# Performance work log

Hardware: AMD Instinct MI355X
Metric: run time of the kernel (lower is better)

Reference implementation:

```python
import jax, jax.numpy as jnp
import numpy as np

B, T, H, OUT_LEN, D_IN, D_OUT = 512, 512, 256, 8, 64, 64

def _lstm_seq(x, Wih, Whh, bih, bhh):
    # batch_first LSTM, zero initial state; x: [B,T,D] -> [B,T,H]
    b = bih + bhh
    h0 = jnp.zeros((x.shape[0], Whh.shape[1]), x.dtype)
    def step(carry, xt):
        h, c = carry
        g = xt @ Wih.T + h @ Whh.T + b
        i, f, gg, o = jnp.split(g, 4, axis=-1)  # torch gate order i,f,g,o
        c = jax.nn.sigmoid(f) * c + jax.nn.sigmoid(i) * jnp.tanh(gg)
        h = jax.nn.sigmoid(o) * jnp.tanh(c)
        return (h, c), h
    _, hs = jax.lax.scan(step, (h0, h0), jnp.swapaxes(x, 0, 1))
    return jnp.swapaxes(hs, 0, 1)

def _lstm_cell0(xt, Wih, bih, bhh):
    # single decode step; original calls self.dec with fresh zero (h,c) each
    # step, so the recurrent matrix Whh never contributes.
    g = xt @ Wih.T + bih + bhh
    i, f, gg, o = jnp.split(g, 4, axis=-1)
    c = jax.nn.sigmoid(i) * jnp.tanh(gg)
    return jax.nn.sigmoid(o) * jnp.tanh(c)

def _mlp(x, Ws, bs, Wl, bl):
    # simple.mlp: hidden Linear+ReLU stack, linear output (dropout off)
    for k in range(Ws.shape[0]):
        x = jax.nn.relu(x @ Ws[k] + bs[k])
    return x @ Wl + bl

def setup_inputs():
    key = jax.random.key(0)
    ks = iter(jax.random.split(key, 32))
    def W(shape, fan):
        return jax.random.normal(next(ks), shape, jnp.float32) / np.float32(np.sqrt(fan))
    return {
        'x': jax.random.normal(next(ks), (B, T, D_IN), jnp.float32),
        'in_W': W((D_IN, H), D_IN), 'in_b': jnp.zeros((H,), jnp.float32),
        'enc_Wih': W((4*H, H), H), 'enc_Whh': W((4*H, H), H),
        'enc_bih': jnp.zeros((4*H,), jnp.float32), 'enc_bhh': jnp.zeros((4*H,), jnp.float32),
        'dec_Wih': W((4*H, 2*H), 2*H), 'dec_Whh': W((4*H, H), H),
        'dec_bih': jnp.zeros((4*H,), jnp.float32), 'dec_bhh': jnp.zeros((4*H,), jnp.float32),
        'w_Ws': W((3, H, H), H), 'w_bs': jnp.zeros((3, H), jnp.float32), 'w_Wl': W((H, H), H), 'w_bl': jnp.zeros((H,), jnp.float32),
        'u_Ws': W((3, H, H), H), 'u_bs': jnp.zeros((3, H), jnp.float32), 'u_Wl': W((H, H), H), 'u_bl': jnp.zeros((H,), jnp.float32),
        'v_Ws': W((7, H, H), H), 'v_bs': jnp.zeros((7, H), jnp.float32), 'v_Wl': W((H, 1), H), 'v_bl': jnp.zeros((1,), jnp.float32),
        'out_W': W((H, D_OUT), H), 'out_b': jnp.zeros((D_OUT,), jnp.float32),
    }

def reference(x, in_W, in_b, enc_Wih, enc_Whh, enc_bih, enc_bhh,
              dec_Wih, dec_Whh, dec_bih, dec_bhh,
              w_Ws, w_bs, w_Wl, w_bl, u_Ws, u_bs, u_Wl, u_bl,
              v_Ws, v_bs, v_Wl, v_bl, out_W, out_b):
    h = x @ in_W + in_b                                       # input projection [B,T,H]
    enc = _lstm_seq(h, enc_Wih, enc_Whh, enc_bih, enc_bhh)    # [B,T,H]
    whs = _mlp(enc, w_Ws, w_bs, w_Wl, w_bl)                   # w(hs), loop-invariant (hoisted)
    def dec_step(s, _):
        us = _mlp(s, u_Ws, u_bs, u_Wl, u_bl)                  # [B,H]
        e = _mlp(jnp.tanh(us[:, None, :] + whs), v_Ws, v_bs, v_Wl, v_bl)  # [B,T,1]
        a = jax.nn.softmax(e, axis=1)                         # softmax over time
        c_t = jnp.sum(a * enc, axis=1)                        # [B,H] weighted sum
        s_new = _lstm_cell0(jnp.concatenate([c_t, s], axis=-1), dec_Wih, dec_bih, dec_bhh)
        return s_new, s_new
    s0 = jnp.zeros((x.shape[0], H), x.dtype)
    _, ss = jax.lax.scan(dec_step, s0, None, length=OUT_LEN)  # [OUT_LEN,B,H]
    dec = jnp.swapaxes(ss, 0, 1)                              # [B,OUT_LEN,H]
    return dec @ out_W + out_b                                # output projection
```

## Files before the change

kernel.cpp:

```cpp
#include <hip/hip_runtime.h>
#include <math.h>

#define B_    512
#define T_    512
#define H_    256
#define DIN_  64
#define OL_   8
#define DOUT_ 64

#define CBv   128
#define HSTR  32768

typedef unsigned short u16;
typedef unsigned int u32;
typedef unsigned long long ull;
typedef __attribute__((ext_vector_type(8))) short short8;
typedef __attribute__((ext_vector_type(4))) float f32x4;

static __device__ __forceinline__ float sigm(float x){ return 1.0f/(1.0f + expf(-x)); }
static __device__ __forceinline__ float bf2f(u16 h){
  u32 u = ((u32)h) << 16; float f; __builtin_memcpy(&f, &u, 4); return f;
}
static __device__ __forceinline__ u16 f2bf(float f){
  u32 u; __builtin_memcpy(&u, &f, 4);
  u = (u + 0x7fffu + ((u >> 16) & 1u)) >> 16;
  return (u16)u;
}
static __device__ __forceinline__ u32 packhl(float f){
  u16 h = f2bf(f);
  u16 lo = f2bf(f - bf2f(h));
  return ((u32)h << 16) | (u32)lo;
}
static __device__ __forceinline__ float unpackhl(u32 w){
  return bf2f((u16)(w >> 16)) + bf2f((u16)(w & 0xffff));
}
static __device__ __forceinline__ u32 al(const u32* p){
  return __hip_atomic_load(p, __ATOMIC_RELAXED, __HIP_MEMORY_SCOPE_AGENT);
}
static __device__ __forceinline__ void as_(u32* p, u32 v){
  __hip_atomic_store(p, v, __ATOMIC_RELAXED, __HIP_MEMORY_SCOPE_AGENT);
}

__global__ void k_wpt(const float* __restrict__ inW, const float* __restrict__ Wih,
                      float* __restrict__ WpT)
{
  int gid = blockIdx.x * 256 + threadIdx.x;
  int c = gid >> 6, d = gid & 63;
  const float* wr = Wih + c * H_;
  const float* ir = inW + d * H_;
  float acc = 0.f;
  #pragma unroll 4
  for (int e = 0; e < H_; e += 4) {
    float4 av = *(const float4*)(ir + e);
    float4 bv = *(const float4*)(wr + e);
    acc += av.x*bv.x + av.y*bv.y + av.z*bv.z + av.w*bv.w;
  }
  WpT[c*64 + d] = acc;
}

__global__ void k_bp(const float* __restrict__ inb, const float* __restrict__ Wih,
                     const float* __restrict__ bih, const float* __restrict__ bhh,
                     float* __restrict__ bp)
{
  int c = blockIdx.x * 256 + threadIdx.x;
  const float* wr = Wih + c * H_;
  float acc = bih[c] + bhh[c];
  for (int e = 0; e < H_; ++e) acc += inb[e] * wr[e];
  bp[c] = acc;
}

__global__ void k_dwt(const float* __restrict__ dWih, float* __restrict__ dWt)
{
  int gid = blockIdx.x * 256 + threadIdx.x;
  int j = gid >> 9, k = gid & 511;
  int row = (j < 256) ? j : (j + 256);
  dWt[k*768 + j] = dWih[row*512 + k];
}

__global__ void k_wall(const float* __restrict__ wWs, const float* __restrict__ wWl,
                       const float* __restrict__ uWs, const float* __restrict__ uWl,
                       const float* __restrict__ vWs, u16* __restrict__ outb)
{
  int lyr = blockIdx.y;
  const float* W = (lyr < 3)  ? wWs + lyr*65536
                 : (lyr == 3) ? wWl
                 : (lyr < 7)  ? uWs + (lyr-4)*65536
                 : (lyr == 7) ? uWl
                 :              vWs + (lyr-8)*65536;
  u16* out = outb + (size_t)lyr*131072;
  int gid = blockIdx.x * 256 + threadIdx.x;
  int k = gid & 255, n = gid >> 8;
  float v = W[k*256 + n];
  int s = k >> 5, j = k & 7;
  int lane = (((k >> 3) & 3) << 4) | (n & 15);
  int fl = ((s*16) + (n >> 4))*512 + lane*8 + j;
  u16 h = f2bf(v);
  out[fl] = h;
  out[65536 + fl] = f2bf(v - bf2f(h));
}

__global__ void k_whhfl(const float* __restrict__ Whh, u16* __restrict__ out)
{
  int gid = blockIdx.x * 256 + threadIdx.x;
  int j = gid & 7, l = (gid >> 3) & 63, ctg = (gid >> 9) & 63, s = gid >> 15;
  int k = s*32 + (l >> 4)*8 + j;
  int wv = ctg >> 2, g = ctg & 3;
  int row = g*256 + wv*16 + (l & 15);
  float v = Whh[row*256 + k];
  int fl = (s*64 + ctg)*512 + l*8 + j;
  u16 h = f2bf(v);
  out[fl] = h;
  out[262144 + fl] = f2bf(v - bf2f(h));
}

__global__ void k_wpfl(const float* __restrict__ WpT, u16* __restrict__ out)
{
  int gid = blockIdx.x * 256 + threadIdx.x;
  int j = gid & 7, l = (gid >> 3) & 63, ctg = (gid >> 9) & 63, s = gid >> 15;
  int k = s*32 + (l >> 4)*8 + j;
  int wv = ctg >> 2, g = ctg & 3;
  int row = g*256 + wv*16 + (l & 15);
  float v = WpT[row*64 + k];
  int fl = (s*64 + ctg)*512 + l*8 + j;
  u16 h = f2bf(v);
  out[fl] = h;
  out[65536 + fl] = f2bf(v - bf2f(h));
}

__global__ __launch_bounds__(256,1) void k_enc(
    const float* __restrict__ x, const u16* __restrict__ whhFL,
    const u16* __restrict__ wpFL, const float* __restrict__ bp,
    u32* __restrict__ henc)
{
  __shared__ float G[2][16][32][4];
  const int tid = threadIdx.x, l = tid & 63, wv = tid >> 6;
  const int lr = l & 15, lk = l >> 4;
  const int rg = blockIdx.x, bg = blockIdx.y, z = blockIdx.z;
  const int ug2 = wv >> 1;
  const int g0 = (wv & 1) * 2;
  const int u16g = bg*2 + ug2;

  short8 whH[8][2], whL[8][2], wpH[2][2], wpL[2][2];
  #pragma unroll
  for (int s = 0; s < 8; ++s)
    #pragma unroll
    for (int c = 0; c < 2; ++c) {
      int ctg = u16g*4 + g0 + c;
      whH[s][c] = *(const short8*)(whhFL + ((size_t)(s*64 + ctg))*512 + l*8);
      whL[s][c] = *(const short8*)(whhFL + 262144 + ((size_t)(s*64 + ctg))*512 + l*8);
    }
  #pragma unroll
  for (int s = 0; s < 2; ++s)
    #pragma unroll
    for (int c = 0; c < 2; ++c) {
      int ctg = u16g*4 + g0 + c;
      wpH[s][c] = *(const short8*)(wpFL + ((size_t)(s*64 + ctg))*512 + l*8);
      wpL[s][c] = *(const short8*)(wpFL + 65536 + ((size_t)(s*64 + ctg))*512 + l*8);
    }
  const int ul = tid & 31, er0 = tid >> 5;
  float bb[4];
  #pragma unroll
  for (int g = 0; g < 4; ++g) bb[g] = bp[g*256 + bg*32 + ul];
  float cs[2] = {0.f, 0.f};

  u32* hz = henc + (size_t)z * (size_t)(T_+1) * HSTR;
  const float* xrow = x + ((size_t)(z*CBv + rg*16 + lr)*T_)*DIN_ + lk*8;

  for (int t = 0; t < T_; ++t) {
    float4 xv0 = *(const float4*)(xrow);
    float4 xv1 = *(const float4*)(xrow + 4);
    float4 xv2 = *(const float4*)(xrow + 32);
    float4 xv3 = *(const float4*)(xrow + 36);
    xrow += DIN_;

    const ull* hb = (const ull*)(hz + (size_t)t*HSTR + (size_t)(rg*16 + lr)*256);
    ull hq[8][4];
    #pragma unroll
    for (int s = 0; s < 8; ++s)
      #pragma unroll
      for (int q = 0; q < 4; ++q)
        hq[s][q] = __hip_atomic_load(hb + s*16 + lk*4 + q,
                                     __ATOMIC_RELAXED, __HIP_MEMORY_SCOPE_AGENT);
    if (t) {
      for (;;) {
        bool ok = true;
        #pragma unroll
        for (int s = 0; s < 8; ++s)
          #pragma unroll
          for (int q = 0; q < 4; ++q) {
            u32 a = (u32)hq[s][q], b = (u32)(hq[s][q] >> 32);
            ok = ok && (a != 0u) && (b != 0u);
          }
        if (__all(ok)) break;
        __builtin_amdgcn_s_sleep(1);
        #pragma unroll
        for (int s = 0; s < 8; ++s)
          #pragma unroll
          for (int q = 0; q < 4; ++q)
            hq[s][q] = __hip_atomic_load(hb + s*16 + lk*4 + q,
                                         __ATOMIC_RELAXED, __HIP_MEMORY_SCOPE_AGENT);
      }
    }

    f32x4 acc[2];
    acc[0] = (f32x4){0.f,0.f,0.f,0.f};
    acc[1] = (f32x4){0.f,0.f,0.f,0.f};

    #pragma unroll
    for (int s = 0; s < 2; ++s) {
      float vv[8];
      if (s == 0) { vv[0]=xv0.x;vv[1]=xv0.y;vv[2]=xv0.z;vv[3]=xv0.w;vv[4]=xv1.x;vv[5]=xv1.y;vv[6]=xv1.z;vv[7]=xv1.w; }
      else        { vv[0]=xv2.x;vv[1]=xv2.y;vv[2]=xv2.z;vv[3]=xv2.w;vv[4]=xv3.x;vv[5]=xv3.y;vv[6]=xv3.z;vv[7]=xv3.w; }
      short8 ah, al2;
      #pragma unroll
      for (int j = 0; j < 8; ++j) {
        u16 h = f2bf(vv[j]);
        ah[j] = (short)h;
        al2[j] = (short)f2bf(vv[j] - bf2f(h));
      }
      #pragma unroll
      for (int c = 0; c < 2; ++c) {
        acc[c] = __builtin_amdgcn_mfma_f32_16x16x32_bf16(ah,  wpH[s][c], acc[c], 0,0,0);
        acc[c] = __builtin_amdgcn_mfma_f32_16x16x32_bf16(al2, wpH[s][c], acc[c], 0,0,0);
        acc[c] = __builtin_amdgcn_mfma_f32_16x16x32_bf16(ah,  wpL[s][c], acc[c], 0,0,0);
      }
    }
    #pragma unroll
    for (int s = 0; s < 8; ++s) {
      short8 ah, al2;
      #pragma unroll
      for (int q = 0; q < 4; ++q) {
        u32 w0 = (u32)hq[s][q], w1 = (u32)(hq[s][q] >> 32);
        ah[q*2]   = (short)(w0 >> 16); al2[q*2]   = (short)(w0 & 0xffff);
        ah[q*2+1] = (short)(w1 >> 16); al2[q*2+1] = (short)(w1 & 0xffff);
      }
      #pragma unroll
      for (int c = 0; c < 2; ++c) {
        acc[c] = __builtin_amdgcn_mfma_f32_16x16x32_bf16(ah,  whH[s][c], acc[c], 0,0,0);
        acc[c] = __builtin_amdgcn_mfma_f32_16x16x32_bf16(al2, whH[s][c], acc[c], 0,0,0);
        acc[c] = __builtin_amdgcn_mfma_f32_16x16x32_bf16(ah,  whL[s][c], acc[c], 0,0,0);
      }
    }

    const int p = t & 1;
    #pragma unroll
    for (int c = 0; c < 2; ++c)
      #pragma unroll
      for (int j = 0; j < 4; ++j)
        G[p][lk*4 + j][ug2*16 + lr][g0 + c] = acc[c][j];
    __syncthreads();

    #pragma unroll
    for (int pp = 0; pp < 2; ++pp) {
      int row = er0 + pp*8;
      float4 gq = *(const float4*)&G[p][row][ul][0];
      float gi = gq.x + bb[0], gf = gq.y + bb[1];
      float gg = gq.z + bb[2], go = gq.w + bb[3];
      float cn = sigm(gf)*cs[pp] + sigm(gi)*tanhf(gg);
      float hn = sigm(go)*tanhf(cn);
      cs[pp] = cn;
      as_(hz + (size_t)(t+1)*HSTR + (size_t)(rg*16 + row)*256 + bg*32 + ul,
          packhl(hn) | 1u);
    }
  }
}

static __device__ __forceinline__ void mlp_core(
    u32* act, const u16* wFL, const float* bs, const float* bl,
    int L, int nbs, bool lastRelu, int tid)
{
  const int l = tid & 63, w = tid >> 6;
  const int rg = w >> 2, cg = w & 3;
  const int lr = l & 15, lk = l >> 4;
  const int wrow = rg*32;
  f32x4 acc[2][4];
  for (int lyr = 0; lyr < L; ++lyr) {
    __syncthreads();
    const u16* wb = wFL + (size_t)lyr*131072;
    #pragma unroll
    for (int rt = 0; rt < 2; ++rt)
      #pragma unroll
      for (int ct = 0; ct < 4; ++ct) acc[rt][ct] = (f32x4){0.f,0.f,0.f,0.f};

    short8 bh[2][4], blo[2][4];
    #pragma unroll
    for (int ct = 0; ct < 4; ++ct) {
      const u16* bfp = wb + ((size_t)(cg*4 + ct))*512 + l*8;
      bh[0][ct]  = *(const short8*)bfp;
      blo[0][ct] = *(const short8*)(bfp + 65536);
    }
    #pragma unroll
    for (int s = 0; s < 8; ++s) {
      const int pb = s & 1, nb = pb ^ 1;
      if (s < 7) {
        #pragma unroll
        for (int ct = 0; ct < 4; ++ct) {
          const u16* bfp = wb + ((size_t)((s+1)*16 + cg*4 + ct))*512 + l*8;
          bh[nb][ct]  = *(const short8*)bfp;
          blo[nb][ct] = *(const short8*)(bfp + 65536);
        }
      }
      short8 ah[2], al2[2];
      #pragma unroll
      for (int rt = 0; rt < 2; ++rt) {
        int row = wrow + rt*16 + lr;
        int cc = s*8 + lk*2;
        const u32* base = act + row*256;
        uint4 d0 = *(const uint4*)(base + (((cc    ) ^ (row & 7)) << 2));
        uint4 d1 = *(const uint4*)(base + (((cc + 1) ^ (row & 7)) << 2));
        u32 q[8] = {d0.x,d0.y,d0.z,d0.w,d1.x,d1.y,d1.z,d1.w};
        #pragma unroll
        for (int j = 0; j < 8; ++j) {
          ah[rt][j]  = (short)(q[j] >> 16);
          al2[rt][j] = (short)(q[j] & 0xffff);
        }
      }
      #pragma unroll
      for (int ct = 0; ct < 4; ++ct)
        #pragma unroll
        for (int rt = 0; rt < 2; ++rt) {
          acc[rt][ct] = __builtin_amdgcn_mfma_f32_16x16x32_bf16(ah[rt],  bh[pb][ct],  acc[rt][ct], 0,0,0);
          acc[rt][ct] = __builtin_amdgcn_mfma_f32_16x16x32_bf16(al2[rt], bh[pb][ct],  acc[rt][ct], 0,0,0);
          acc[rt][ct] = __builtin_amdgcn_mfma_f32_16x16x32_bf16(ah[rt],  blo[pb][ct], acc[rt][ct], 0,0,0);
        }
    }
    const float* bptr = (lyr < nbs) ? (bs + lyr*256) : bl;
    const bool dorelu = (lyr < L-1) || lastRelu;
    #pragma unroll
    for (int ct = 0; ct < 4; ++ct) {
      float bv = bptr[cg*64 + ct*16 + lr];
      #pragma unroll
      for (int rt = 0; rt < 2; ++rt)
        #pragma unroll
        for (int g = 0; g < 4; ++g) {
          float xv = acc[rt][ct][g] + bv;
          acc[rt][ct][g] = dorelu ? fmaxf(xv, 0.f) : xv;
        }
    }
    __syncthreads();
    #pragma unroll
    for (int ct = 0; ct < 4; ++ct) {
      int n = cg*64 + ct*16 + lr;
      #pragma unroll
      for (int rt = 0; rt < 2; ++rt)
        #pragma unroll
        for (int g = 0; g < 4; ++g) {
          int row = wrow + rt*16 + lk*4 + g;
          act[row*256 + (((n >> 2) ^ (row & 7)) << 2) + (n & 3)] = packhl(acc[rt][ct][g]);
        }
    }
  }
  __syncthreads();
}

__global__ __launch_bounds__(512,1) void k_dec_all(
    const u32* __restrict__ henc, const u16* __restrict__ mlpFL,
    const float* __restrict__ wbs, const float* __restrict__ wbl,
    const float* __restrict__ ubs, const float* __restrict__ ubl,
    const float* __restrict__ vbs, const float* __restrict__ vWl,
    const float* __restrict__ vbl,
    const float* __restrict__ dWt, const float* __restrict__ dbih,
    const float* __restrict__ dbhh,
    const float* __restrict__ oW, const float* __restrict__ ob,
    u32* __restrict__ whsP, u32* __restrict__ usb, u32* __restrict__ usflag,
    u32* __restrict__ eS, u32* __restrict__ ctxS, u32* __restrict__ sS,
    float* __restrict__ outc)
{
  extern __shared__ u32 act[];
  __shared__ float red[8], red2[8];
  const int bid = blockIdx.x, tid = threadIdx.x;
  const u16* wFLw = mlpFL;
  const u16* wFLu = mlpFL + 4*131072;
  const u16* wFLv = mlpFL + 8*131072;
  float sprev[4] = {0.f, 0.f, 0.f, 0.f};

  for (int k = 0; k < 4; ++k) {
    long m0t = (long)(bid + 256*k) * 64;
    __syncthreads();
    for (int i = tid; i < 4096; i += 512) {
      int row = i >> 6, c16 = i & 63;
      long m = m0t + row;
      uint4 pk = *(const uint4*)(henc + HSTR + m*256 + c16*4);
      *((uint4*)(act + row*256 + ((c16 ^ (row & 7)) << 2))) = pk;
    }
    mlp_core(act, wFLw, wbs, wbl, 4, 3, false, tid);
    for (int i = tid; i < 4096; i += 512) {
      int row = i >> 6, c16 = i & 63;
      long m = m0t + row;
      uint4 pk = *((const uint4*)(act + row*256 + ((c16 ^ (row & 7)) << 2)));
      *(uint4*)(whsP + m*256 + c16*4) = pk;
    }
  }

  for (int s = 0; s < OL_; ++s) {
    if (bid < 2) {
      long m0t = (long)bid * 64;
      __syncthreads();
      for (int i = tid; i < 4096; i += 512) {
        int row = i >> 6, c16 = i & 63;
        const u32* sp = sS + (size_t)s*32768 + (m0t + row)*256 + c16*4;
        u32 w0 = al(sp), w1 = al(sp+1), w2 = al(sp+2), w3 = al(sp+3);
        if (s) {
          while (!(w0 && w1 && w2 && w3)) {
            __builtin_amdgcn_s_sleep(1);
            w0 = al(sp); w1 = al(sp+1); w2 = al(sp+2); w3 = al(sp+3);
          }
        }
        uint4 pk = { packhl(__uint_as_float(w0)), packhl(__uint_as_float(w1)),
                     packhl(__uint_as_float(w2)), packhl(__uint_as_float(w3)) };
        *((uint4*)(act + row*256 + ((c16 ^ (row & 7)) << 2))) = pk;
      }
      mlp_core(act, wFLu, ubs, ubl, 4, 3, false, tid);
      for (int i = tid; i < 4096; i += 512) {
        int row = i >> 6, c16 = i & 63;
        uint4 pk = *((const uint4*)(act + row*256 + ((c16 ^ (row & 7)) << 2)));
        *(uint4*)(usb + (size_t)s*32768 + (m0t + row)*256 + c16*4) = pk;
      }
      __syncthreads();
      if (tid == 0)
        __hip_atomic_store(usflag + s*2 + bid, 1u,
                           __ATOMIC_RELEASE, __HIP_MEMORY_SCOPE_AGENT);
    }

    {
      if (tid < 64) {
        const u32* f0 = usflag + s*2;
        for (;;) {
          u32 a0 = al(f0), a1 = al(f0 + 1);
          if (a0 & a1) break;
          __builtin_amdgcn_s_sleep(2);
        }
      }
      __syncthreads();
      __builtin_amdgcn_fence(__ATOMIC_ACQUIRE, "agent");
    }

    for (int k = 0; k < 4; ++k) {
      long m0t = (long)(bid + 256*k) * 64;
      __syncthreads();
      for (int i = tid; i < 4096; i += 512) {
        int row = i >> 6, c16 = i & 63;
        long m = m0t + row;
        uint4 pw = *(const uint4*)(whsP + m*256 + c16*4);
        uint4 uw = *(const uint4*)(usb + (size_t)s*32768 + (m & 127)*256 + c16*4);
        uint4 pk;
        pk.x = packhl(tanhf(unpackhl(pw.x) + unpackhl(uw.x)));
        pk.y = packhl(tanhf(unpackhl(pw.y) + unpackhl(uw.y)));
        pk.z = packhl(tanhf(unpackhl(pw.z) + unpackhl(uw.z)));
        pk.w = packhl(tanhf(unpackhl(pw.w) + unpackhl(uw.w)));
        *((uint4*)(act + row*256 + ((c16 ^ (row & 7)) << 2))) = pk;
      }
      mlp_core(act, wFLv, vbs, vbs, 7, 7, true, tid);
      {
        int r2 = tid >> 3, q = tid & 7;
        float p = 0.f;
        #pragma unroll 8
        for (int j = 0; j < 32; ++j) {
          int n = q*32 + j;
          u32 w = act[r2*256 + (((n >> 2) ^ (r2 & 7)) << 2) + (n & 3)];
          p += unpackhl(w) * vWl[n];
        }
        p += __shfl_xor(p, 1, 64);
        p += __shfl_xor(p, 2, 64);
        p += __shfl_xor(p, 4, 64);
        if (q == 0)
          as_(eS + (size_t)s*65536 + m0t + r2, __float_as_uint(p + vbl[0]) | 1u);
      }
    }

    if (bid >= 64 && bid < 192) {
      int b = bid - 64;
      __syncthreads();
      float* asx = (float*)act;
      const u32* ep0 = eS + (size_t)s*65536 + b;
      u32 w0;
      for (;;) {
        w0 = al(ep0 + (size_t)tid*128);
        if (w0) break;
        __builtin_amdgcn_s_sleep(1);
      }
      float v0 = __uint_as_float(w0);
      const int lane = tid & 63, wv = tid >> 6;
      float m = v0;
      #pragma unroll
      for (int o = 32; o; o >>= 1) m = fmaxf(m, __shfl_xor(m, o, 64));
      if (!lane) red[wv] = m;
      __syncthreads();
      m = fmaxf(fmaxf(fmaxf(red[0], red[1]), fmaxf(red[2], red[3])),
                fmaxf(fmaxf(red[4], red[5]), fmaxf(red[6], red[7])));
      float x0 = expf(v0 - m);
      float sm = x0;
      #pragma unroll
      for (int o = 32; o; o >>= 1) sm += __shfl_xor(sm, o, 64);
      if (!lane) red2[wv] = sm;
      __syncthreads();
      float inv = 1.f / (red2[0] + red2[1] + red2[2] + red2[3]
                       + red2[4] + red2[5] + red2[6] + red2[7]);
      asx[tid] = x0 * inv;
      __syncthreads();
      int unit = tid & 255, half = tid >> 8;
      float accv = 0.f;
      const u32* hp = henc + HSTR + (size_t)b*256 + unit;
      #pragma unroll 8
      for (int t = half*256; t < half*256 + 256; ++t)
        accv += asx[t] * unpackhl(hp[(size_t)t*HSTR]);
      float* part = asx + 512;
      part[tid] = accv;
      __syncthreads();
      if (half == 0)
        as_(ctxS + (size_t)s*32768 + b*256 + unit,
            __float_as_uint(accv + part[256 + unit]) | 1u);
    }

    if (bid >= 224) {
      int c = bid - 224, b0r = c*4;
      __syncthreads();
      float* xt = (float*)act;
      const int u = tid & 255, kh = tid >> 8;
      if (kh == 0) {
        const u32* cp = ctxS + (size_t)s*32768 + (size_t)b0r*256 + u;
        u32 w0, w1, w2, w3;
        for (;;) {
          w0 = al(cp); w1 = al(cp + 256); w2 = al(cp + 512); w3 = al(cp + 768);
          if (w0 && w1 && w2 && w3) break;
          __builtin_amdgcn_s_sleep(1);
        }
        xt[0*520 + u] = __uint_as_float(w0);
        xt[1*520 + u] = __uint_as_float(w1);
        xt[2*520 + u] = __uint_as_float(w2);
        xt[3*520 + u] = __uint_as_float(w3);
        #pragma unroll
        for (int bb = 0; bb < 4; ++bb) xt[bb*520 + 256 + u] = sprev[bb];
      }
      __syncthreads();
      float ai[4], ag[4], ao[4];
      #pragma unroll
      for (int bb = 0; bb < 4; ++bb) { ai[bb]=0.f; ag[bb]=0.f; ao[bb]=0.f; }
      #pragma unroll 4
      for (int k = kh*256; k < kh*256 + 256; ++k) {
        float wi = dWt[k*768 + u];
        float wg = dWt[k*768 + 256 + u];
        float wo = dWt[k*768 + 512 + u];
        #pragma unroll
        for (int bb = 0; bb < 4; ++bb) {
          float xv = xt[bb*520 + k];
          ai[bb] += xv*wi; ag[bb] += xv*wg; ao[bb] += xv*wo;
        }
      }
      float* pr = xt + 4*520;
      if (kh) {
        #pragma unroll
        for (int bb = 0; bb < 4; ++bb) {
          pr[(0*4 + bb)*256 + u] = ai[bb];
          pr[(1*4 + bb)*256 + u] = ag[bb];
          pr[(2*4 + bb)*256 + u] = ao[bb];
        }
      }
      __syncthreads();
      float* sn = pr + 3*4*256;
      if (!kh) {
        float bi = dbih[u]       + dbhh[u];
        float bg = dbih[512 + u] + dbhh[512 + u];
        float bo = dbih[768 + u] + dbhh[768 + u];
        #pragma unroll
        for (int bb = 0; bb < 4; ++bb) {
          float a1 = ai[bb] + pr[(0*4 + bb)*256 + u];
          float g1 = ag[bb] + pr[(1*4 + bb)*256 + u];
          float o1 = ao[bb] + pr[(2*4 + bb)*256 + u];
          float cn = sigm(a1 + bi) * tanhf(g1 + bg);
          float hn = sigm(o1 + bo) * tanhf(cn);
          as_(sS + (size_t)(s+1)*32768 + (size_t)(b0r + bb)*256 + u,
              __float_as_uint(hn) | 1u);
          sprev[bb] = hn;
          sn[bb*256 + u] = hn;
        }
      }
      __syncthreads();
      if (tid < 256) {
        int d = tid & 63, rr = tid >> 6;
        float a2 = ob[d];
        #pragma unroll 4
        for (int k = 0; k < 256; ++k) a2 += sn[rr*256 + k] * oW[k*64 + d];
        outc[((size_t)(b0r + rr)*OL_ + s)*64 + d] = a2;
      }
    }
  }
  (void)wFLw;
}

extern "C" void kernel_launch(void* const* d_in, const int* in_sizes, int n_in,
                              void* d_out, int out_size, void* d_ws, size_t ws_size,
                              hipStream_t stream)
{
  (void)in_sizes; (void)n_in;
  const float* x    = (const float*)d_in[0];
  const float* inW  = (const float*)d_in[1];
  const float* inb  = (const float*)d_in[2];
  const float* eWih = (const float*)d_in[3];
  const float* eWhh = (const float*)d_in[4];
  const float* ebih = (const float*)d_in[5];
  const float* ebhh = (const float*)d_in[6];
  const float* dWih = (const float*)d_in[7];
  const float* dbih = (const float*)d_in[9];
  const float* dbhh = (const float*)d_in[10];
  const float* wWs  = (const float*)d_in[11];
  const float* wbs  = (const float*)d_in[12];
  const float* wWl  = (const float*)d_in[13];
  const float* wbl  = (const float*)d_in[14];
  const float* uWs  = (const float*)d_in[15];
  const float* ubs  = (const float*)d_in[16];
  const float* uWl  = (const float*)d_in[17];
  const float* ubl  = (const float*)d_in[18];
  const float* vWs  = (const float*)d_in[19];
  const float* vbs  = (const float*)d_in[20];
  const float* vWl  = (const float*)d_in[21];
  const float* vbl  = (const float*)d_in[22];
  const float* oW   = (const float*)d_in[23];
  const float* ob   = (const float*)d_in[24];
  float* out = (float*)d_out;

  hipFuncSetAttribute((const void*)k_dec_all, hipFuncAttributeMaxDynamicSharedMemorySize, 65536);

  const size_t hsz = (size_t)(T_+1) * HSTR;
  const size_t avail = ws_size / 4;
  auto needf = [&](int nc) -> size_t {
    return (size_t)nc*hsz + 16777216ull  + 1343552ull
         + 1770496ull  + 4096;
  };
  int NC = (needf(2) <= avail) ? 2 : 1;
  if (needf(NC) > avail) { hipMemsetAsync(d_out, 0, (size_t)out_size*4, stream); return; }

  float* wsf = (float*)d_ws;
  size_t o = 0;
  u32* henc = (u32*)(wsf + o);  o += (size_t)NC*hsz;
  u32* whsP = (u32*)(wsf + o);  o += 16777216;
  u32* usb  = (u32*)(wsf + o);  o += 262144;
  u32* usflag = (u32*)(wsf + o); o += 64;
  u32* eS   = (u32*)(wsf + o);  o += 524288;
  u32* ctxS = (u32*)(wsf + o);  o += 262144;
  u32* sS   = (u32*)(wsf + o);  o += 294912;
  float* WpT = wsf + o;  o += 65536;
  float* bp  = wsf + o;  o += 1024;
  float* dWt = wsf + o;  o += 393216;
  u16* whhFL = (u16*)(wsf + o);  o += 262144;
  u16* wpFL  = (u16*)(wsf + o);  o += 65536;
  u16* mlpFL = (u16*)(wsf + o);

  const size_t scratchBytes = (262144ull + 64 + 524288 + 262144 + 294912) * 4;

  k_wpt<<<256, 256, 0, stream>>>(inW, eWih, WpT);
  k_bp <<<4,   256, 0, stream>>>(inb, eWih, ebih, ebhh, bp);
  k_dwt<<<1536,256, 0, stream>>>(dWih, dWt);
  k_whhfl<<<1024,256,0,stream>>>(eWhh, whhFL);
  k_wpfl <<<256, 256,0,stream>>>(WpT, wpFL);
  k_wall <<<dim3(256,15), 256, 0, stream>>>(wWs, wWl, uWs, uWl, vWs, mlpFL);

  for (int c0 = 0; c0 < B_; c0 += CBv*NC) {
    hipMemsetAsync(henc, 0, (size_t)NC*hsz*4, stream);

    k_enc<<<dim3(CBv/16, 8, NC), 256, 0, stream>>>(
        x + (size_t)c0*T_*DIN_, whhFL, wpFL, bp, henc);

    for (int z = 0; z < NC; ++z) {
      hipMemsetAsync(usb, 0, scratchBytes, stream);
      k_dec_all<<<256, 512, 65536, stream>>>(
          henc + (size_t)z*hsz, mlpFL,
          wbs, wbl, ubs, ubl, vbs, vWl, vbl,
          dWt, dbih, dbhh, oW, ob,
          whsP, usb, usflag, eS, ctxS, sS,
          out + (size_t)(c0 + z*CBv)*OL_*DOUT_);
    }
  }
}
```

Before: 18.63 ms.

## Recompute w-MLP per decode step and compute u-MLP per block in LDS

Drops the precomputed whs buffer in global memory and recomputes the w-MLP projection of the encoder states inside every decode step. The result is fused directly with the tanh(u+w) activation in LDS. Each block also computes its own half of the u-MLP redundantly into a second LDS buffer, which removes the two-block producer step and the global flag spin-wait. The cost is much more matrix work per step (the 4-layer w-MLP runs eight times instead of once, plus a redundant u-MLP in every block) and double the dynamic shared memory.

```diff
diff --git a/kernel.cpp b/kernel.cpp
--- a/kernel.cpp
+++ b/kernel.cpp
@@ -362,78 +362,40 @@
     const float* __restrict__ dWt, const float* __restrict__ dbih,
     const float* __restrict__ dbhh,
     const float* __restrict__ oW, const float* __restrict__ ob,
-    u32* __restrict__ whsP, u32* __restrict__ usb, u32* __restrict__ usflag,
     u32* __restrict__ eS, u32* __restrict__ ctxS, u32* __restrict__ sS,
     float* __restrict__ outc)
 {
   extern __shared__ u32 act[];
   __shared__ float red[8], red2[8];
   const int bid = blockIdx.x, tid = threadIdx.x;
+  u32* usL = act + 16384;
   const u16* wFLw = mlpFL;
   const u16* wFLu = mlpFL + 4*131072;
   const u16* wFLv = mlpFL + 8*131072;
+  const int half = bid & 1;
   float sprev[4] = {0.f, 0.f, 0.f, 0.f};
 
-  for (int k = 0; k < 4; ++k) {
-    long m0t = (long)(bid + 256*k) * 64;
+  for (int s = 0; s < OL_; ++s) {
     __syncthreads();
     for (int i = tid; i < 4096; i += 512) {
       int row = i >> 6, c16 = i & 63;
-      long m = m0t + row;
-      uint4 pk = *(const uint4*)(henc + HSTR + m*256 + c16*4);
+      uint4 pk;
+      if (s) {
+        const u32* sp = sS + (size_t)s*32768 + (size_t)(half*64 + row)*256 + c16*4;
+        u32 w0 = al(sp), w1 = al(sp+1), w2 = al(sp+2), w3 = al(sp+3);
+        while (!(w0 && w1 && w2 && w3)) {
+          __builtin_amdgcn_s_sleep(1);
+          w0 = al(sp); w1 = al(sp+1); w2 = al(sp+2); w3 = al(sp+3);
+        }
+        pk = (uint4){ packhl(__uint_as_float(w0)), packhl(__uint_as_float(w1)),
+                      packhl(__uint_as_float(w2)), packhl(__uint_as_float(w3)) };
+      } else {
+        pk = (uint4){0u, 0u, 0u, 0u};
+      }
       *((uint4*)(act + row*256 + ((c16 ^ (row & 7)) << 2))) = pk;
     }
-    mlp_core(act, wFLw, wbs, wbl, 4, 3, false, tid);
-    for (int i = tid; i < 4096; i += 512) {
-      int row = i >> 6, c16 = i & 63;
-      long m = m0t + row;
-      uint4 pk = *((const uint4*)(act + row*256 + ((c16 ^ (row & 7)) << 2)));
-      *(uint4*)(whsP + m*256 + c16*4) = pk;
-    }
-  }
-
-  for (int s = 0; s < OL_; ++s) {
-    if (bid < 2) {
-      long m0t = (long)bid * 64;
-      __syncthreads();
-      for (int i = tid; i < 4096; i += 512) {
-        int row = i >> 6, c16 = i & 63;
-        const u32* sp = sS + (size_t)s*32768 + (m0t + row)*256 + c16*4;
-        u32 w0 = al(sp), w1 = al(sp+1), w2 = al(sp+2), w3 = al(sp+3);
-        if (s) {
-          while (!(w0 && w1 && w2 && w3)) {
-            __builtin_amdgcn_s_sleep(1);
-            w0 = al(sp); w1 = al(sp+1); w2 = al(sp+2); w3 = al(sp+3);
-          }
-        }
-        uint4 pk = { packhl(__uint_as_float(w0)), packhl(__uint_as_float(w1)),
-                     packhl(__uint_as_float(w2)), packhl(__uint_as_float(w3)) };
-        *((uint4*)(act + row*256 + ((c16 ^ (row & 7)) << 2))) = pk;
-      }
-      mlp_core(act, wFLu, ubs, ubl, 4, 3, false, tid);
-      for (int i = tid; i < 4096; i += 512) {
-        int row = i >> 6, c16 = i & 63;
-        uint4 pk = *((const uint4*)(act + row*256 + ((c16 ^ (row & 7)) << 2)));
-        *(uint4*)(usb + (size_t)s*32768 + (m0t + row)*256 + c16*4) = pk;
-      }
-      __syncthreads();
-      if (tid == 0)
-        __hip_atomic_store(usflag + s*2 + bid, 1u,
-                           __ATOMIC_RELEASE, __HIP_MEMORY_SCOPE_AGENT);
-    }
-
-    {
-      if (tid < 64) {
-        const u32* f0 = usflag + s*2;
-        for (;;) {
-          u32 a0 = al(f0), a1 = al(f0 + 1);
-          if (a0 & a1) break;
-          __builtin_amdgcn_s_sleep(2);
-        }
-      }
-      __syncthreads();
-      __builtin_amdgcn_fence(__ATOMIC_ACQUIRE, "agent");
-    }
+    mlp_core(act, wFLu, ubs, ubl, 4, 3, false, tid);
+    for (int i = tid; i < 16384; i += 512) usL[i] = act[i];
 
     for (int k = 0; k < 4; ++k) {
       long m0t = (long)(bid + 256*k) * 64;
@@ -441,14 +403,13 @@
       for (int i = tid; i < 4096; i += 512) {
         int row = i >> 6, c16 = i & 63;
         long m = m0t + row;
-        uint4 pw = *(const uint4*)(whsP + m*256 + c16*4);
-        uint4 uw = *(const uint4*)(usb + (size_t)s*32768 + (m & 127)*256 + c16*4);
-        uint4 pk;
-        pk.x = packhl(tanhf(unpackhl(pw.x) + unpackhl(uw.x)));
-        pk.y = packhl(tanhf(unpackhl(pw.y) + unpackhl(uw.y)));
-        pk.z = packhl(tanhf(unpackhl(pw.z) + unpackhl(uw.z)));
-        pk.w = packhl(tanhf(unpackhl(pw.w) + unpackhl(uw.w)));
+        uint4 pk = *(const uint4*)(henc + HSTR + m*256 + c16*4);
         *((uint4*)(act + row*256 + ((c16 ^ (row & 7)) << 2))) = pk;
+      }
+      mlp_core(act, wFLw, wbs, wbl, 4, 3, false, tid);
+      for (int i = tid; i < 16384; i += 512) {
+        u32 a = act[i], u = usL[i];
+        act[i] = packhl(tanhf(unpackhl(a) + unpackhl(u)));
       }
       mlp_core(act, wFLv, vbs, vbs, 7, 7, true, tid);
       {
@@ -498,16 +459,16 @@
                        + red2[4] + red2[5] + red2[6] + red2[7]);
       asx[tid] = x0 * inv;
       __syncthreads();
-      int unit = tid & 255, half = tid >> 8;
+      int unit = tid & 255, hf = tid >> 8;
       float accv = 0.f;
       const u32* hp = henc + HSTR + (size_t)b*256 + unit;
       #pragma unroll 8
-      for (int t = half*256; t < half*256 + 256; ++t)
+      for (int t = hf*256; t < hf*256 + 256; ++t)
         accv += asx[t] * unpackhl(hp[(size_t)t*HSTR]);
       float* part = asx + 512;
       part[tid] = accv;
       __syncthreads();
-      if (half == 0)
+      if (hf == 0)
         as_(ctxS + (size_t)s*32768 + b*256 + unit,
             __float_as_uint(accv + part[256 + unit]) | 1u);
     }
@@ -585,7 +546,6 @@
       }
     }
   }
-  (void)wFLw;
 }
 
 extern "C" void kernel_launch(void* const* d_in, const int* in_sizes, int n_in,
@@ -619,13 +579,15 @@
   const float* ob   = (const float*)d_in[24];
   float* out = (float*)d_out;
 
-  hipFuncSetAttribute((const void*)k_dec_all, hipFuncAttributeMaxDynamicSharedMemorySize, 65536);
+  hipFuncSetAttribute((const void*)k_dec_all, hipFuncAttributeMaxDynamicSharedMemorySize, 131072);
 
   const size_t hsz = (size_t)(T_+1) * HSTR;
   const size_t avail = ws_size / 4;
   auto needf = [&](int nc) -> size_t {
-    return (size_t)nc*hsz + 16777216ull  + 1343552ull
-         + 1770496ull  + 4096;
+    return (size_t)nc*hsz
+         + 1081344ull
+         + 1770496ull
+         + 4096;
   };
   int NC = (needf(2) <= avail) ? 2 : 1;
   if (needf(NC) > avail) { hipMemsetAsync(d_out, 0, (size_t)out_size*4, stream); return; }
@@ -633,9 +595,6 @@
   float* wsf = (float*)d_ws;
   size_t o = 0;
   u32* henc = (u32*)(wsf + o);  o += (size_t)NC*hsz;
-  u32* whsP = (u32*)(wsf + o);  o += 16777216;
-  u32* usb  = (u32*)(wsf + o);  o += 262144;
-  u32* usflag = (u32*)(wsf + o); o += 64;
   u32* eS   = (u32*)(wsf + o);  o += 524288;
   u32* ctxS = (u32*)(wsf + o);  o += 262144;
   u32* sS   = (u32*)(wsf + o);  o += 294912;
@@ -646,7 +605,7 @@
   u16* wpFL  = (u16*)(wsf + o);  o += 65536;
   u16* mlpFL = (u16*)(wsf + o);
 
-  const size_t scratchBytes = (262144ull + 64 + 524288 + 262144 + 294912) * 4;
+  const size_t scratchBytes = (524288ull + 262144 + 294912) * 4;
 
   k_wpt<<<256, 256, 0, stream>>>(inW, eWih, WpT);
   k_bp <<<4,   256, 0, stream>>>(inb, eWih, ebih, ebhh, bp);
@@ -662,12 +621,12 @@
         x + (size_t)c0*T_*DIN_, whhFL, wpFL, bp, henc);
 
     for (int z = 0; z < NC; ++z) {
-      hipMemsetAsync(usb, 0, scratchBytes, stream);
-      k_dec_all<<<256, 512, 65536, stream>>>(
+      hipMemsetAsync(eS, 0, scratchBytes, stream);
+      k_dec_all<<<256, 512, 131072, stream>>>(
           henc + (size_t)z*hsz, mlpFL,
           wbs, wbl, ubs, ubl, vbs, vWl, vbl,
           dWt, dbih, dbhh, oW, ob,
-          whsP, usb, usflag, eS, ctxS, sS,
+          eS, ctxS, sS,
           out + (size_t)(c0 + z*CBv)*OL_*DOUT_);
     }
   }
```

New measurement: 21.41 ms. 14.9% more time.
